# Kernel tuning notes

Measured on AMD Instinct MI355X. Metric: run time of the kernel, lower is better.

The kernel has to match this reference:

```python
import jax, jax.numpy as jnp
import numpy as np

TOKENS, HIDDEN, N_EXPERTS = 16384, 2048, 64
JITTER_EPS = 0.01
Z_LOSS_COEFF = 0.001


def setup_inputs() -> dict:
    key = jax.random.key(0)
    k1, k2 = jax.random.split(key)
    x = jax.random.normal(k1, (TOKENS, HIDDEN), dtype=jnp.float32)
    w = jax.random.normal(k2, (N_EXPERTS, HIDDEN), dtype=jnp.float32) * 0.02  # router weight [E,H]
    return {"x": x, "w": w}


def _route_pass(scores_sel, scores, jitter_eps):
    # scores_sel: logits possibly with -inf at already-selected expert (top-2 pass)
    # scores:     original logits (used for abs/clamp factor, as in torch code)
    mx = jnp.max(scores_sel, axis=-1, keepdims=True)                      # [N,1]
    factor = jnp.maximum(jnp.abs(scores), mx)                             # scores.abs().clamp(min=mx)
    mask = jax.lax.stop_gradient((mx - scores) / factor > 2.0 * jitter_eps)
    masked_logits = jnp.where(mask, -jnp.inf, scores_sel)
    # eval path (training=False): selected_experts = argmax of (masked-for-selection) scores
    sel = jnp.argmax(scores_sel, axis=-1)[..., None]                      # [N,1] int
    gates = jax.nn.softmax(masked_logits, axis=-1)
    # mask_for_one: selected == argmax(gates) holds deterministically in eval -> 1.0
    mult = jnp.take_along_axis(gates, sel, axis=-1)                       # [N,1]
    return mult, sel


def reference(x, w):
    logits = x @ w.T                                                      # [N,E]
    # z-loss (identity on logits in forward; scalar returned for completeness)
    z_loss = Z_LOSS_COEFF * jnp.mean(jnp.square(jax.nn.logsumexp(logits, axis=-1)))
    original_gates = jax.nn.softmax(logits, axis=-1)
    # top-1 pass
    m1, s1 = _route_pass(logits, logits, JITTER_EPS)
    # top-2 pass: mask out the first selection
    e_idx = jnp.arange(logits.shape[-1])[None, :]
    scores2 = jnp.where(e_idx == s1, -jnp.inf, logits)
    m2, s2 = _route_pass(scores2, logits, JITTER_EPS)
    multiplier = jnp.concatenate([m1, m2], axis=-1)                       # [N,2]
    selected_experts = jnp.concatenate([s1, s2], axis=-1)                 # [N,2]
    return multiplier, original_gates, selected_experts, z_loss
```

## Files before the change

kernel.cpp:

```cpp
#include <hip/hip_runtime.h>
#include <math.h>

#define TOKENS 16384
#define HIDDEN 2048
#define NEXP   64
#define MT     64
#define NBLK   (TOKENS / MT)
#define CK     128
#define NCH    (HIDDEN / CK)
#define XCB    8192
#define BUFB   65536

#define GATES_OFF (TOKENS * 2)
#define SEL_OFF   (GATES_OFF + TOKENS * NEXP)
#define Z_OFF     (SEL_OFF + TOKENS * 2)

#define WIMG_BYTES (NEXP * HIDDEN * 2 * 2)

typedef __attribute__((ext_vector_type(8))) _Float16 f16x8;
typedef __attribute__((ext_vector_type(4))) float    f32x4;

__device__ __forceinline__ float wave_sum64(float v) {
    #pragma unroll
    for (int s = 1; s < 64; s <<= 1) v += __shfl_xor(v, s, 64);
    return v;
}

__device__ __forceinline__ void dma16(const void* g, void* l) {
    __builtin_amdgcn_global_load_lds(
        (const __attribute__((address_space(1))) unsigned int*)g,
        (__attribute__((address_space(3))) unsigned int*)l, 16, 0, 0);
}

__global__ __launch_bounds__(256) void wconvert(
    const float* __restrict__ w, uint4* __restrict__ wimg)
{
    const int s = blockIdx.x * 256 + threadIdx.x;
    const int c    = s >> 10;
    const int r    = s & 1023;
    const int l    = r & 63;
    const int nt   = (r >> 6) & 1;
    const int kh   = (r >> 7) & 1;
    const int term = (r >> 8) & 1;
    const int eh   = (r >> 9) & 1;
    const int e = eh * 32 + nt * 16 + (l & 15);
    const int k = c * 64 + kh * 32 + (l >> 4) * 8;

    const float* src = w + (size_t)e * HIDDEN + k;
    union { _Float16 f[8]; uint4 u; } o;
    #pragma unroll
    for (int j = 0; j < 8; ++j) {
        const float v = src[j];
        const _Float16 h = (_Float16)v;
        o.f[j] = (term == 0) ? h : (_Float16)((v - (float)h) * 4096.f);
    }
    wimg[s] = o.u;
}

__device__ __forceinline__ void cvt_split(const float4 a, const float4 b,
                                          f16x8& hi, f16x8& lo) {
    union { _Float16 f[8]; f16x8 v; } H, L;
    #pragma unroll
    for (int j = 0; j < 4; ++j) {
        const float s0 = (&a.x)[j];
        const float s1 = (&b.x)[j];
        const _Float16 h0 = (_Float16)s0;
        const _Float16 h1 = (_Float16)s1;
        H.f[j]     = h0;
        H.f[j + 4] = h1;
        L.f[j]     = (_Float16)((s0 - (float)h0) * 4096.f);
        L.f[j + 4] = (_Float16)((s1 - (float)h1) * 4096.f);
    }
    hi = H.v; lo = L.v;
}

__global__ __launch_bounds__(256, 1) void router_main(
    const float* __restrict__ x, const uint4* __restrict__ wimg,
    float* __restrict__ out, float* __restrict__ zpartial)
{
    __shared__ __align__(16) unsigned char smem[2 * BUFB];
    __shared__ float zred[4];

    const int tid  = threadIdx.x;
    const int wv   = __builtin_amdgcn_readfirstlane(tid >> 6);
    const int lane = tid & 63;
    const int rowr = lane & 15;
    const int kg   = lane >> 4;
    const int t0b  = blockIdx.x * MT;

    const float* xq = x + (size_t)(t0b + wv * 16 + rowr) * HIDDEN + kg * 4;
    const uint4* wB = wimg + lane;

    f32x4 acc0[4], acc1[4];
    #pragma unroll
    for (int g = 0; g < 4; ++g) { acc0[g] = (f32x4)0.f; acc1[g] = (f32x4)0.f; }

    {
        unsigned char* xd = smem + wv * XCB;
        #pragma unroll
        for (int j = 0; j < 8; ++j)
            dma16(xq + j * 16, xd + j * 1024);
        unsigned char* bd = smem + 32768;
        #pragma unroll
        for (int i = 0; i < 8; ++i) {
            const int m = wv * 8 + i;
            dma16(wB + m * 64, bd + m * 1024);
        }
    }
    __syncthreads();

    #pragma unroll 2
    for (int c = 0; c < NCH; ++c) {
        const int buf = c & 1;

        if (c + 1 < NCH) {
            unsigned char* xd = smem + (buf ^ 1) * BUFB + wv * XCB;
            #pragma unroll
            for (int j = 0; j < 8; ++j)
                dma16(xq + (c + 1) * CK + j * 16, xd + j * 1024);
            unsigned char* bd = smem + (buf ^ 1) * BUFB + 32768;
            #pragma unroll
            for (int i = 0; i < 8; ++i) {
                const int m = wv * 8 + i;
                dma16(wB + (size_t)(c + 1) * 2048 + m * 64, bd + m * 1024);
            }
        }

        const unsigned char* xb = smem + buf * BUFB + wv * XCB + kg * 512 + rowr * 16;
        const unsigned char* bb = smem + buf * BUFB + 32768;
        #pragma unroll
        for (int s = 0; s < 4; ++s) {
            const int pb = ((s >> 1) * 1024 + (s & 1) * 128 + lane) * 16;
            f16x8 bh[4], bl[4];
            bh[0] = *(const f16x8*)(bb + pb);
            bh[1] = *(const f16x8*)(bb + pb + 64 * 16);
            bh[2] = *(const f16x8*)(bb + pb + 512 * 16);
            bh[3] = *(const f16x8*)(bb + pb + 576 * 16);
            bl[0] = *(const f16x8*)(bb + pb + 256 * 16);
            bl[1] = *(const f16x8*)(bb + pb + 320 * 16);
            bl[2] = *(const f16x8*)(bb + pb + 768 * 16);
            bl[3] = *(const f16x8*)(bb + pb + 832 * 16);

            const float4 va = *(const float4*)(xb + s * 2048);
            const float4 vb = *(const float4*)(xb + s * 2048 + 256);
            f16x8 Ah, Al;
            cvt_split(va, vb, Ah, Al);
            #pragma unroll
            for (int g = 0; g < 4; ++g) {
                acc0[g] = __builtin_amdgcn_mfma_f32_16x16x32_f16(Ah, bh[g], acc0[g], 0, 0, 0);
                acc1[g] = __builtin_amdgcn_mfma_f32_16x16x32_f16(Ah, bl[g], acc1[g], 0, 0, 0);
                acc1[g] = __builtin_amdgcn_mfma_f32_16x16x32_f16(Al, bh[g], acc1[g], 0, 0, 0);
            }
        }

        __syncthreads();
    }

    float zsum = 0.f;
    #pragma unroll
    for (int r = 0; r < 4; ++r) {
        const int t = wv * 16 + kg * 4 + r;
        float v[4]; int e[4];
        #pragma unroll
        for (int g = 0; g < 4; ++g) {
            v[g] = acc0[g][r] + acc1[g][r] * (1.f / 4096.f);
            e[g] = g * 16 + rowr;
        }

        float bv = v[0]; int bi = e[0];
        #pragma unroll
        for (int g = 1; g < 4; ++g)
            if (v[g] > bv) { bv = v[g]; bi = e[g]; }
        #pragma unroll
        for (int st = 1; st < 16; st <<= 1) {
            const float ov = __shfl_xor(bv, st, 64);
            const int   oi = __shfl_xor(bi, st, 64);
            if (ov > bv || (ov == bv && oi < bi)) { bv = ov; bi = oi; }
        }
        const float max1 = bv; const int s1 = bi;

        float e1[4], se = 0.f, sm1 = 0.f;
        #pragma unroll
        for (int g = 0; g < 4; ++g) {
            e1[g] = expf(v[g] - max1);
            se += e1[g];
            const bool m1 = (max1 - v[g]) > 0.02f * fmaxf(fabsf(v[g]), max1);
            sm1 += m1 ? 0.f : e1[g];
        }
        #pragma unroll
        for (int st = 1; st < 16; st <<= 1) {
            se  += __shfl_xor(se, st, 64);
            sm1 += __shfl_xor(sm1, st, 64);
        }

        #pragma unroll
        for (int g = 0; g < 4; ++g)
            out[GATES_OFF + (size_t)(t0b + t) * NEXP + e[g]] = e1[g] / se;

        const float lse = max1 + logf(se);
        if (rowr == 0) zsum += lse * lse;

        float bv2 = (e[0] == s1) ? -INFINITY : v[0]; int bi2 = e[0];
        #pragma unroll
        for (int g = 1; g < 4; ++g) {
            const float cv = (e[g] == s1) ? -INFINITY : v[g];
            if (cv > bv2) { bv2 = cv; bi2 = e[g]; }
        }
        #pragma unroll
        for (int st = 1; st < 16; st <<= 1) {
            const float ov = __shfl_xor(bv2, st, 64);
            const int   oi = __shfl_xor(bi2, st, 64);
            if (ov > bv2 || (ov == bv2 && oi < bi2)) { bv2 = ov; bi2 = oi; }
        }
        const float max2 = bv2; const int s2 = bi2;

        float sm2 = 0.f;
        #pragma unroll
        for (int g = 0; g < 4; ++g) {
            const bool m2 = (max2 - v[g]) > 0.02f * fmaxf(fabsf(v[g]), max2);
            sm2 += (m2 || e[g] == s1) ? 0.f : expf(v[g] - max2);
        }
        #pragma unroll
        for (int st = 1; st < 16; st <<= 1)
            sm2 += __shfl_xor(sm2, st, 64);

        if (rowr == 0) {
            const size_t trow = (size_t)(t0b + t) * 2;
            out[trow + 0] = 1.f / sm1;
            out[trow + 1] = 1.f / sm2;
            out[SEL_OFF + trow + 0] = (float)s1;
            out[SEL_OFF + trow + 1] = (float)s2;
        }
    }

    const float zt = wave_sum64(zsum);
    if (lane == 0) zred[wv] = zt;
    __syncthreads();
    if (tid == 0)
        zpartial[blockIdx.x] = zred[0] + zred[1] + zred[2] + zred[3];
}

__global__ __launch_bounds__(256) void zfinal(
    const float* __restrict__ zpartial, float* __restrict__ out)
{
    const int tid = threadIdx.x;
    float v = zpartial[tid];
    v = wave_sum64(v);
    __shared__ float red[4];
    if ((tid & 63) == 0) red[tid >> 6] = v;
    __syncthreads();
    if (tid == 0) {
        const float tot = red[0] + red[1] + red[2] + red[3];
        out[Z_OFF] = 0.001f * (tot / (float)TOKENS);
    }
}

extern "C" void kernel_launch(void* const* d_in, const int* in_sizes, int n_in,
                              void* d_out, int out_size, void* d_ws, size_t ws_size,
                              hipStream_t stream) {
    const float* x = (const float*)d_in[0];
    const float* w = (const float*)d_in[1];
    float* out = (float*)d_out;

    uint4* wimg     = (uint4*)d_ws;
    float* zpartial = (float*)((char*)d_ws + WIMG_BYTES);

    wconvert<<<128, 256, 0, stream>>>(w, wimg);
    router_main<<<NBLK, 256, 0, stream>>>(x, wimg, out, zpartial);
    zfinal<<<1, 256, 0, stream>>>(zpartial, out);
}
```

Baseline: 221.6 us.

## Deepen load pipeline to four-slot ring with explicit vmcnt waits

Splits the K loop into 64-wide chunks and stages them through a four-slot LDS ring, keeping three chunks of async global-to-LDS loads in flight. Each iteration waits with hand-counted s_waitcnt vmcnt values and a single raw s_barrier, replacing the double buffer and its two __syncthreads per chunk. The goal is to hide global memory latency behind MFMA work. The hand-tuned vmcnt counts are fragile and depend on the assumed per-chunk load count, and the B-operand reads move into the inner loop, interleaved with the MFMAs.

```diff
diff --git a/kernel.cpp b/kernel.cpp
--- a/kernel.cpp
+++ b/kernel.cpp
@@ -6,10 +6,10 @@
 #define NEXP   64
 #define MT     64
 #define NBLK   (TOKENS / MT)
-#define CK     128
+#define CK     64
 #define NCH    (HIDDEN / CK)
-#define XCB    8192
-#define BUFB   65536
+#define SLOT   32768
+#define BOFF   16384
 
 #define GATES_OFF (TOKENS * 2)
 #define SEL_OFF   (GATES_OFF + TOKENS * NEXP)
@@ -74,11 +74,25 @@
     hi = H.v; lo = L.v;
 }
 
+__device__ __forceinline__ void stage_chunk(
+    unsigned char* smem, const float* xq, const uint4* wq, int wv, int c)
+{
+    unsigned char* s = smem + (size_t)(c & 3) * SLOT;
+    unsigned char* xd = s + wv * 4096;
+    #pragma unroll
+    for (int j = 0; j < 4; ++j)
+        dma16(xq + c * CK + j * 16, xd + j * 1024);
+    unsigned char* bd = s + BOFF + wv * 4096;
+    #pragma unroll
+    for (int i = 0; i < 4; ++i)
+        dma16(wq + (size_t)c * 1024 + i * 64, bd + i * 1024);
+}
+
 __global__ __launch_bounds__(256, 1) void router_main(
     const float* __restrict__ x, const uint4* __restrict__ wimg,
     float* __restrict__ out, float* __restrict__ zpartial)
 {
-    __shared__ __align__(16) unsigned char smem[2 * BUFB];
+    __shared__ __align__(16) unsigned char smem[4 * SLOT];
     __shared__ float zred[4];
 
     const int tid  = threadIdx.x;
@@ -89,71 +103,50 @@
     const int t0b  = blockIdx.x * MT;
 
     const float* xq = x + (size_t)(t0b + wv * 16 + rowr) * HIDDEN + kg * 4;
-    const uint4* wB = wimg + lane;
+    const uint4* wq = wimg + wv * 256 + lane;
 
     f32x4 acc0[4], acc1[4];
     #pragma unroll
     for (int g = 0; g < 4; ++g) { acc0[g] = (f32x4)0.f; acc1[g] = (f32x4)0.f; }
 
-    {
-        unsigned char* xd = smem + wv * XCB;
-        #pragma unroll
-        for (int j = 0; j < 8; ++j)
-            dma16(xq + j * 16, xd + j * 1024);
-        unsigned char* bd = smem + 32768;
-        #pragma unroll
-        for (int i = 0; i < 8; ++i) {
-            const int m = wv * 8 + i;
-            dma16(wB + m * 64, bd + m * 1024);
-        }
-    }
-    __syncthreads();
-
-    #pragma unroll 2
+    stage_chunk(smem, xq, wq, wv, 0);
+    stage_chunk(smem, xq, wq, wv, 1);
+    stage_chunk(smem, xq, wq, wv, 2);
+
     for (int c = 0; c < NCH; ++c) {
-        const int buf = c & 1;
-
-        if (c + 1 < NCH) {
-            unsigned char* xd = smem + (buf ^ 1) * BUFB + wv * XCB;
-            #pragma unroll
-            for (int j = 0; j < 8; ++j)
-                dma16(xq + (c + 1) * CK + j * 16, xd + j * 1024);
-            unsigned char* bd = smem + (buf ^ 1) * BUFB + 32768;
-            #pragma unroll
-            for (int i = 0; i < 8; ++i) {
-                const int m = wv * 8 + i;
-                dma16(wB + (size_t)(c + 1) * 2048 + m * 64, bd + m * 1024);
-            }
-        }
-
-        const unsigned char* xb = smem + buf * BUFB + wv * XCB + kg * 512 + rowr * 16;
-        const unsigned char* bb = smem + buf * BUFB + 32768;
-        #pragma unroll
-        for (int s = 0; s < 4; ++s) {
-            const int pb = ((s >> 1) * 1024 + (s & 1) * 128 + lane) * 16;
-            f16x8 bh[4], bl[4];
-            bh[0] = *(const f16x8*)(bb + pb);
-            bh[1] = *(const f16x8*)(bb + pb + 64 * 16);
-            bh[2] = *(const f16x8*)(bb + pb + 512 * 16);
-            bh[3] = *(const f16x8*)(bb + pb + 576 * 16);
-            bl[0] = *(const f16x8*)(bb + pb + 256 * 16);
-            bl[1] = *(const f16x8*)(bb + pb + 320 * 16);
-            bl[2] = *(const f16x8*)(bb + pb + 768 * 16);
-            bl[3] = *(const f16x8*)(bb + pb + 832 * 16);
-
-            const float4 va = *(const float4*)(xb + s * 2048);
-            const float4 vb = *(const float4*)(xb + s * 2048 + 256);
+        if (c < NCH - 2) {
+            asm volatile("s_waitcnt vmcnt(16)" ::: "memory");
+        } else if (c == NCH - 2) {
+            asm volatile("s_waitcnt vmcnt(8)" ::: "memory");
+        } else {
+            asm volatile("s_waitcnt vmcnt(0)" ::: "memory");
+        }
+        __builtin_amdgcn_sched_barrier(0);
+        asm volatile("s_barrier" ::: "memory");
+        __builtin_amdgcn_sched_barrier(0);
+
+        if (c + 3 < NCH) stage_chunk(smem, xq, wq, wv, c + 3);
+
+        const unsigned char* s  = smem + (size_t)(c & 3) * SLOT;
+        const unsigned char* xw = s + wv * 4096;
+        const unsigned char* bw = s + BOFF;
+        #pragma unroll
+        for (int kh = 0; kh < 2; ++kh) {
+            const int kb = (2 * kh + (kg >> 1)) * 1024 + (kg & 1) * 512 + rowr * 16;
+            const float4 va = *(const float4*)(xw + kb);
+            const float4 vb = *(const float4*)(xw + kb + 256);
             f16x8 Ah, Al;
             cvt_split(va, vb, Ah, Al);
             #pragma unroll
             for (int g = 0; g < 4; ++g) {
-                acc0[g] = __builtin_amdgcn_mfma_f32_16x16x32_f16(Ah, bh[g], acc0[g], 0, 0, 0);
-                acc1[g] = __builtin_amdgcn_mfma_f32_16x16x32_f16(Ah, bl[g], acc1[g], 0, 0, 0);
-                acc1[g] = __builtin_amdgcn_mfma_f32_16x16x32_f16(Al, bh[g], acc1[g], 0, 0, 0);
+                const int sh = ((g >> 1) * 512 + kh * 128 + (g & 1) * 64 + lane) * 16;
+                const f16x8 bh = *(const f16x8*)(bw + sh);
+                const f16x8 bl = *(const f16x8*)(bw + sh + 4096);
+                acc0[g] = __builtin_amdgcn_mfma_f32_16x16x32_f16(Ah, bh, acc0[g], 0, 0, 0);
+                acc1[g] = __builtin_amdgcn_mfma_f32_16x16x32_f16(Ah, bl, acc1[g], 0, 0, 0);
+                acc1[g] = __builtin_amdgcn_mfma_f32_16x16x32_f16(Al, bh, acc1[g], 0, 0, 0);
             }
         }
-
-        __syncthreads();
     }
 
     float zsum = 0.f;
```

After: 216.7 us. 1.02x faster.
